# Kernel tuning notes

Measured on AMD Instinct MI355X. Metric: run time of the kernel, lower is better.

The kernel has to match this reference:

```python
import jax, jax.numpy as jnp
import numpy as np

GROUPS = 32
EPS = 1e-5


def group_norm(x, scale, bias):
    # x: [B, C, T]
    b, c, t = x.shape
    xg = x.reshape(b, GROUPS, c // GROUPS, t)
    mean = xg.mean(axis=(2, 3), keepdims=True)
    var = xg.var(axis=(2, 3), keepdims=True)
    xg = (xg - mean) * jax.lax.rsqrt(var + EPS)
    return xg.reshape(b, c, t) * scale[None, :, None] + bias[None, :, None]


def setup_inputs() -> dict:
    key = jax.random.key(0)
    ks = jax.random.split(key, 7)
    B, C, H, W = 8, 512, 32, 32
    x = jax.random.normal(ks[0], (B, C, H, W), dtype=jnp.float32)
    gn_scale = jnp.ones((C,), jnp.float32)
    gn_bias = jnp.zeros((C,), jnp.float32)
    qkv_w = jax.random.normal(ks[1], (3 * C, C), jnp.float32) / np.sqrt(C)
    qkv_b = jnp.zeros((3 * C,), jnp.float32)
    # proj_out is zero-initialized in the original; use small random weights
    # so the attention path contributes to the output (trained-model behavior).
    proj_w = jax.random.normal(ks[2], (C, C), jnp.float32) / np.sqrt(C)
    proj_b = jnp.zeros((C,), jnp.float32)
    return {"x": x, "gn_scale": gn_scale, "gn_bias": gn_bias,
            "qkv_w": qkv_w, "qkv_b": qkv_b, "proj_w": proj_w, "proj_b": proj_b}


def reference(x, gn_scale, gn_bias, qkv_w, qkv_b, proj_w, proj_b):
    NUM_HEADS = 8
    b, c, *spatial = x.shape
    t = int(np.prod(spatial))
    xf = x.reshape(b, c, t)                                   # [B,C,T]
    xn = group_norm(xf, gn_scale, gn_bias)
    qkv = jnp.einsum('oc,bct->bot', qkv_w, xn) + qkv_b[None, :, None]  # [B,3C,T]
    # legacy layout: reshape to heads BEFORE splitting into q,k,v thirds
    qkv = qkv.reshape(b * NUM_HEADS, -1, t)                   # [B*H, 3C/H, T]
    ch = qkv.shape[1] // 3
    q, k, v = jnp.split(qkv, 3, axis=1)                       # each [B*H, ch, T]
    scale = 1.0 / np.sqrt(np.sqrt(ch))
    w = jnp.einsum('bct,bcs->bts', q * scale, k * scale)      # [B*H, T, T]
    w = jax.nn.softmax(w.astype(jnp.float32), axis=-1).astype(w.dtype)
    h = jnp.einsum('bts,bcs->bct', w, v)                      # [B*H, ch, T]
    h = h.reshape(b, c, t)
    h = jnp.einsum('oc,bct->bot', proj_w, h) + proj_b[None, :, None]
    return (xf + h).reshape(b, c, *spatial)
```

## Files before the change

### kernel.cpp

```cpp
#include <hip/hip_runtime.h>

typedef __bf16 bf16;
typedef __attribute__((ext_vector_type(8))) __bf16 bf16x8;
typedef __attribute__((ext_vector_type(4))) __bf16 bf16x4;
typedef __attribute__((ext_vector_type(4))) float f32x4;

#define MFMA(a, b, c) __builtin_amdgcn_mfma_f32_16x16x32_bf16(a, b, c, 0, 0, 0)
#define GLOAD_LDS(g, l)                                                        \
  __builtin_amdgcn_global_load_lds(                                            \
      (const __attribute__((address_space(1))) void*)(g),                      \
      (__attribute__((address_space(3))) void*)(l), 16, 0, 0)

#if __has_builtin(__builtin_amdgcn_exp2f)
#define EXP2(x) __builtin_amdgcn_exp2f(x)
#else
#define EXP2(x) exp2f(x)
#endif

#define C1LOG 0.18033688011f

__device__ __forceinline__ int swz64(int row, int col) {
  return row * 64 + (col ^ ((row & 7) << 3));
}

__global__ void k_pre(const float* __restrict__ x, const float* __restrict__ gs,
                      const float* __restrict__ gb, const float* __restrict__ qw,
                      const float* __restrict__ pw, bf16* __restrict__ xnT,
                      bf16* __restrict__ wq, bf16* __restrict__ wp) {
  int tid = threadIdx.x;
  __shared__ float red[2][4];
  if (blockIdx.x >= 256) {
    int i = (blockIdx.x - 256) * 256 + tid;
    int idx = i * 4;
    float4 v;
    bf16* o;
    if (idx < 786432) {
      v = *(const float4*)(qw + idx);
      o = wq + idx;
    } else {
      int j = idx - 786432;
      v = *(const float4*)(pw + j);
      o = wp + j;
    }
    o[0] = (bf16)v.x; o[1] = (bf16)v.y; o[2] = (bf16)v.z; o[3] = (bf16)v.w;
    return;
  }
  int blk = blockIdx.x;
  int b = blk >> 5, g = blk & 31;
  const float* xp = x + ((size_t)(b * 512 + g * 16)) * 1024;
  float s = 0.f, ss = 0.f;
  for (int i = tid; i < 4096; i += 256) {
    float4 v = ((const float4*)xp)[i];
    s += v.x + v.y + v.z + v.w;
    ss += v.x * v.x + v.y * v.y + v.z * v.z + v.w * v.w;
  }
#pragma unroll
  for (int m = 1; m < 64; m <<= 1) {
    s += __shfl_xor(s, m);
    ss += __shfl_xor(ss, m);
  }
  int wid = tid >> 6;
  if ((tid & 63) == 0) { red[0][wid] = s; red[1][wid] = ss; }
  __syncthreads();
  float fs = red[0][0] + red[0][1] + red[0][2] + red[0][3];
  float fss = red[1][0] + red[1][1] + red[1][2] + red[1][3];
  float mean = fs * (1.f / 16384.f);
  float var = fss * (1.f / 16384.f) - mean * mean;
  float inv = rsqrtf(var + 1e-5f);
  float a_[16], b_[16];
#pragma unroll
  for (int cl = 0; cl < 16; ++cl) {
    float sc = gs[g * 16 + cl] * inv;
    a_[cl] = sc;
    b_[cl] = gb[g * 16 + cl] - mean * sc;
  }
  bf16* outp = xnT + (size_t)b * 1024 * 512 + g * 16;
  for (int k = 0; k < 4; ++k) {
    int t = tid + k * 256;
    __align__(16) bf16 tmp[16];
#pragma unroll
    for (int cl = 0; cl < 16; ++cl) {
      float v = xp[(size_t)cl * 1024 + t];
      tmp[cl] = (bf16)(v * a_[cl] + b_[cl]);
    }
    *(bf16x8*)(outp + (size_t)t * 512) = *(bf16x8*)tmp;
    *(bf16x8*)(outp + (size_t)t * 512 + 8) = *(bf16x8*)(tmp + 8);
  }
}

__global__ void k_qkv(const bf16* __restrict__ xnT, const bf16* __restrict__ wq,
                      const float* __restrict__ qb, bf16* __restrict__ qkvT,
                      bf16* __restrict__ vTout) {
  int bid = blockIdx.x;
  int swz = (bid & 7) * 96 + (bid >> 3);
  int nt = swz % 12, mt = swz / 12;
  int tid = threadIdx.x, lane = tid & 63;
  int wid = tid >> 6, wr = wid >> 1, wc = wid & 1;
  int lr = lane & 15, lk8 = (lane >> 4) * 8, prow4 = (lane >> 4) * 4;
  __shared__ __align__(16) bf16 lA[8192], lB[8192];
  const bf16* Ab = xnT + (size_t)mt * 128 * 512;
  const bf16* Bb = wq + (size_t)nt * 128 * 512;
  f32x4 acc[4][4] = {};
  int ubase = tid & 192;
  for (int kt = 0; kt < 8; ++kt) {
    __syncthreads();
#pragma unroll
    for (int i = 0; i < 4; ++i) {
      int s = i * 256 + tid;
      int r = s >> 3, cc = (s & 7) ^ (r & 7);
      GLOAD_LDS(Ab + (size_t)r * 512 + kt * 64 + cc * 8, lA + (i * 256 + ubase) * 8);
      GLOAD_LDS(Bb + (size_t)r * 512 + kt * 64 + cc * 8, lB + (i * 256 + ubase) * 8);
    }
    __syncthreads();
#pragma unroll
    for (int ksl = 0; ksl < 2; ++ksl) {
      bf16x8 aF[4], bF[4];
#pragma unroll
      for (int m = 0; m < 4; ++m)
        aF[m] = *(bf16x8*)&lA[swz64(wr * 64 + m * 16 + lr, ksl * 32 + lk8)];
#pragma unroll
      for (int n = 0; n < 4; ++n)
        bF[n] = *(bf16x8*)&lB[swz64(wc * 64 + n * 16 + lr, ksl * 32 + lk8)];
      __builtin_amdgcn_s_setprio(1);
#pragma unroll
      for (int m = 0; m < 4; ++m)
#pragma unroll
        for (int n = 0; n < 4; ++n) acc[m][n] = MFMA(aF[m], bF[n], acc[m][n]);
      __builtin_amdgcn_s_setprio(0);
    }
  }
#pragma unroll
  for (int n = 0; n < 4; ++n) {
    int o = nt * 128 + wc * 64 + n * 16 + lr;
    float bias = qb[o];
    int hh = o / 192;
    int om = o - hh * 192;
    bool isv = om >= 128;
    float scl = (om >= 64 && om < 128) ? C1LOG : 1.0f;
    int c = om - 128;
#pragma unroll
    for (int m = 0; m < 4; ++m) {
      int row0 = mt * 128 + wr * 64 + m * 16 + prow4;
      if (isv) {
        int bb = row0 >> 10, t0 = row0 & 1023;
        bf16x4 v4;
#pragma unroll
        for (int r = 0; r < 4; ++r) v4[r] = (bf16)(acc[m][n][r] + bias);
        *(bf16x4*)&vTout[(((size_t)bb * 8 + hh) * 64 + c) * 1024 + t0] = v4;
      } else {
#pragma unroll
        for (int r = 0; r < 4; ++r)
          qkvT[(size_t)(row0 + r) * 1536 + o] = (bf16)((acc[m][n][r] + bias) * scl);
      }
    }
  }
}

__global__ __launch_bounds__(512, 4) void k_attn(const bf16* __restrict__ qkvT,
                                                 const bf16* __restrict__ vT,
                                                 bf16* __restrict__ hT) {
  int d = blockIdx.x;
  int head = (d & 7) * 8 + (d >> 6);
  int qt = (d >> 3) & 7;
  int b = head >> 3, hh = head & 7;
  int tid = threadIdx.x, lane = tid & 63, wid = tid >> 6;
  int lr = lane & 15, hi = lane >> 4, lk8 = hi * 8;

  __shared__ __align__(16) bf16 KT[2][4096];
  __shared__ __align__(16) bf16 VTl[2][4096];
  __shared__ __align__(16) bf16 PT[8][1024];

  const bf16* qbase = qkvT + (size_t)b * 1024 * 1536 + hh * 192;
  const bf16* kbase = qbase + 64;
  const bf16* vbase = vT + (size_t)head * 64 * 1024;

  int tq = qt * 128 + wid * 16 + lr;
  bf16x8 qf0 = *(const bf16x8*)(qbase + (size_t)tq * 1536 + lk8);
  bf16x8 qf1 = *(const bf16x8*)(qbase + (size_t)tq * 1536 + 32 + lk8);

  f32x4 hacc[4] = {};
  float m2 = -1e30f, l_ = 0.f;

  int r_ = tid >> 3;
  int cc_ = (tid & 7) ^ (r_ & 7);
  const bf16* ksrc = kbase + (size_t)r_ * 1536 + cc_ * 8;
  const bf16* vsrc = vbase + (size_t)r_ * 1024 + cc_ * 8;
  int lbase = (tid >> 6) * 512;

  GLOAD_LDS(ksrc, KT[0] + lbase);
  GLOAD_LDS(vsrc, VTl[0] + lbase);

  for (int it = 0; it < 16; ++it) {
    int cur = it & 1;
    asm volatile("s_waitcnt vmcnt(0) lgkmcnt(0)" ::: "memory");
    __builtin_amdgcn_s_barrier();
    __builtin_amdgcn_sched_barrier(0);
    if (it < 15) {
      int sb = (it + 1) * 64;
      GLOAD_LDS(ksrc + (size_t)sb * 1536, KT[cur ^ 1] + lbase);
      GLOAD_LDS(vsrc + sb, VTl[cur ^ 1] + lbase);
    }
    f32x4 sc[4];
#pragma unroll
    for (int n = 0; n < 4; ++n) sc[n] = f32x4{0.f, 0.f, 0.f, 0.f};
    __builtin_amdgcn_s_setprio(1);
#pragma unroll
    for (int n = 0; n < 4; ++n) {
      bf16x8 kA0 = *(bf16x8*)&KT[cur][swz64(n * 16 + lr, lk8)];
      bf16x8 kA1 = *(bf16x8*)&KT[cur][swz64(n * 16 + lr, 32 + lk8)];
      sc[n] = MFMA(kA0, qf0, sc[n]);
      sc[n] = MFMA(kA1, qf1, sc[n]);
    }
    __builtin_amdgcn_s_setprio(0);
    float tm = fmaxf(
        fmaxf(fmaxf(fmaxf(sc[0][0], sc[0][1]), fmaxf(sc[0][2], sc[0][3])),
              fmaxf(fmaxf(sc[1][0], sc[1][1]), fmaxf(sc[1][2], sc[1][3]))),
        fmaxf(fmaxf(fmaxf(sc[2][0], sc[2][1]), fmaxf(sc[2][2], sc[2][3])),
              fmaxf(fmaxf(sc[3][0], sc[3][1]), fmaxf(sc[3][2], sc[3][3]))));
    tm = fmaxf(tm, __shfl_xor(tm, 16));
    tm = fmaxf(tm, __shfl_xor(tm, 32));
    if (__any(tm > m2 + 7.213f)) {
      float mn = fmaxf(m2, tm);
      float al = EXP2(m2 - mn);
      m2 = mn;
      l_ *= al;
#pragma unroll
      for (int n = 0; n < 4; ++n) {
        hacc[n][0] *= al; hacc[n][1] *= al; hacc[n][2] *= al; hacc[n][3] *= al;
      }
    }
    float rs = 0.f;
#pragma unroll
    for (int n = 0; n < 4; ++n) {
      float e0 = EXP2(sc[n][0] - m2), e1 = EXP2(sc[n][1] - m2);
      float e2 = EXP2(sc[n][2] - m2), e3 = EXP2(sc[n][3] - m2);
      rs += (e0 + e1) + (e2 + e3);
      bf16x4 p4;
      p4[0] = (bf16)e0; p4[1] = (bf16)e1; p4[2] = (bf16)e2; p4[3] = (bf16)e3;
      *(bf16x4*)&PT[wid][swz64(lr, n * 16 + hi * 4)] = p4;
    }
    rs += __shfl_xor(rs, 16);
    rs += __shfl_xor(rs, 32);
    l_ += rs;
    asm volatile("s_waitcnt lgkmcnt(0)" ::: "memory");
    __builtin_amdgcn_sched_barrier(0);
    bf16x8 pa0 = *(bf16x8*)&PT[wid][swz64(lr, lk8)];
    bf16x8 pa1 = *(bf16x8*)&PT[wid][swz64(lr, 32 + lk8)];
    __builtin_amdgcn_s_setprio(1);
#pragma unroll
    for (int n = 0; n < 4; ++n) {
      bf16x8 vA0 = *(bf16x8*)&VTl[cur][swz64(n * 16 + lr, lk8)];
      bf16x8 vA1 = *(bf16x8*)&VTl[cur][swz64(n * 16 + lr, 32 + lk8)];
      hacc[n] = MFMA(vA0, pa0, hacc[n]);
      hacc[n] = MFMA(vA1, pa1, hacc[n]);
    }
    __builtin_amdgcn_s_setprio(0);
  }
  float invl = 1.f / l_;
  bf16* dst = hT + ((size_t)b * 1024 + tq) * 512 + hh * 64 + hi * 4;
#pragma unroll
  for (int n = 0; n < 4; ++n) {
    bf16x4 o4;
#pragma unroll
    for (int r = 0; r < 4; ++r) o4[r] = (bf16)(hacc[n][r] * invl);
    *(bf16x4*)(dst + n * 16) = o4;
  }
}

__global__ void k_proj(const bf16* __restrict__ hT, const bf16* __restrict__ wp,
                       const float* __restrict__ pb, const float* __restrict__ x,
                       float* __restrict__ out) {
  int bid = blockIdx.x;
  int swz = (bid & 7) * 64 + (bid >> 3);
  int nt = swz & 7, mt = swz >> 3;
  int tid = threadIdx.x, lane = tid & 63;
  int wid = tid >> 6, wr = wid >> 1, wc = wid & 1;
  int lr = lane & 15, lk8 = (lane >> 4) * 8, prow4 = (lane >> 4) * 4;
  __shared__ __align__(16) bf16 lA[8192], lB[4096];
  const bf16* Ab = hT + (size_t)mt * 128 * 512;
  const bf16* Bb = wp + (size_t)nt * 64 * 512;
  f32x4 acc[4][2] = {};
  int ubase = tid & 192;
  for (int kt = 0; kt < 8; ++kt) {
    __syncthreads();
#pragma unroll
    for (int i = 0; i < 4; ++i) {
      int s = i * 256 + tid;
      int r = s >> 3, cc = (s & 7) ^ (r & 7);
      GLOAD_LDS(Ab + (size_t)r * 512 + kt * 64 + cc * 8, lA + (i * 256 + ubase) * 8);
    }
#pragma unroll
    for (int i = 0; i < 2; ++i) {
      int s = i * 256 + tid;
      int r = s >> 3, cc = (s & 7) ^ (r & 7);
      GLOAD_LDS(Bb + (size_t)r * 512 + kt * 64 + cc * 8, lB + (i * 256 + ubase) * 8);
    }
    __syncthreads();
#pragma unroll
    for (int ksl = 0; ksl < 2; ++ksl) {
      bf16x8 aF[4], bF[2];
#pragma unroll
      for (int m = 0; m < 4; ++m)
        aF[m] = *(bf16x8*)&lA[swz64(wr * 64 + m * 16 + lr, ksl * 32 + lk8)];
#pragma unroll
      for (int n = 0; n < 2; ++n)
        bF[n] = *(bf16x8*)&lB[swz64(wc * 32 + n * 16 + lr, ksl * 32 + lk8)];
      __builtin_amdgcn_s_setprio(1);
#pragma unroll
      for (int m = 0; m < 4; ++m)
#pragma unroll
        for (int n = 0; n < 2; ++n) acc[m][n] = MFMA(aF[m], bF[n], acc[m][n]);
      __builtin_amdgcn_s_setprio(0);
    }
  }
#pragma unroll
  for (int n = 0; n < 2; ++n) {
    int o = nt * 64 + wc * 32 + n * 16 + lr;
    float bias = pb[o];
#pragma unroll
    for (int m = 0; m < 4; ++m) {
      int row0 = mt * 128 + wr * 64 + m * 16 + prow4;
      int bb = row0 >> 10, t0 = row0 & 1023;
      size_t off = ((size_t)bb * 512 + o) * 1024 + t0;
      float4 xv = *(const float4*)(x + off);
      float4 rr;
      rr.x = acc[m][n][0] + xv.x + bias;
      rr.y = acc[m][n][1] + xv.y + bias;
      rr.z = acc[m][n][2] + xv.z + bias;
      rr.w = acc[m][n][3] + xv.w + bias;
      *(float4*)(out + off) = rr;
    }
  }
}

extern "C" void kernel_launch(void* const* d_in, const int* in_sizes, int n_in,
                              void* d_out, int out_size, void* d_ws, size_t ws_size,
                              hipStream_t stream) {
  const float* x = (const float*)d_in[0];
  const float* gs = (const float*)d_in[1];
  const float* gb = (const float*)d_in[2];
  const float* qw = (const float*)d_in[3];
  const float* qb = (const float*)d_in[4];
  const float* pw = (const float*)d_in[5];
  const float* pb = (const float*)d_in[6];
  float* out = (float*)d_out;
  char* ws = (char*)d_ws;
  bf16* xnT  = (bf16*)(ws);
  bf16* qkvT = (bf16*)(ws + 8388608);
  bf16* vT   = (bf16*)(ws + 33554432);
  bf16* hT   = (bf16*)(ws + 41943040);
  bf16* wq   = (bf16*)(ws + 50331648);
  bf16* wp   = (bf16*)(ws + 51904512);

  k_pre<<<1280, 256, 0, stream>>>(x, gs, gb, qw, pw, xnT, wq, wp);
  k_qkv<<<768, 256, 0, stream>>>(xnT, wq, qb, qkvT, vT);
  k_attn<<<512, 512, 0, stream>>>(qkvT, vT, hT);
  k_proj<<<512, 256, 0, stream>>>(hT, wp, pb, x, out);
}
```

Baseline: 78.08 us.

## Triple-buffer K/V loads in attention and stage group-norm input through LDS

```diff
diff --git a/kernel.cpp b/kernel.cpp
--- a/kernel.cpp
+++ b/kernel.cpp
@@ -23,12 +23,12 @@
   return row * 64 + (col ^ ((row & 7) << 3));
 }
 
-__global__ void k_pre(const float* __restrict__ x, const float* __restrict__ gs,
-                      const float* __restrict__ gb, const float* __restrict__ qw,
-                      const float* __restrict__ pw, bf16* __restrict__ xnT,
-                      bf16* __restrict__ wq, bf16* __restrict__ wp) {
+__global__ __launch_bounds__(256, 2) void k_pre(
+    const float* __restrict__ x, const float* __restrict__ gs,
+    const float* __restrict__ gb, const float* __restrict__ qw,
+    const float* __restrict__ pw, bf16* __restrict__ xnT,
+    bf16* __restrict__ wq, bf16* __restrict__ wp) {
   int tid = threadIdx.x;
-  __shared__ float red[2][4];
   if (blockIdx.x >= 256) {
     int i = (blockIdx.x - 256) * 256 + tid;
     int idx = i * 4;
@@ -45,12 +45,15 @@
     o[0] = (bf16)v.x; o[1] = (bf16)v.y; o[2] = (bf16)v.z; o[3] = (bf16)v.w;
     return;
   }
+  __shared__ float xs[16 * 1024];
+  __shared__ float red[2][4];
   int blk = blockIdx.x;
   int b = blk >> 5, g = blk & 31;
   const float* xp = x + ((size_t)(b * 512 + g * 16)) * 1024;
   float s = 0.f, ss = 0.f;
   for (int i = tid; i < 4096; i += 256) {
     float4 v = ((const float4*)xp)[i];
+    *(float4*)&xs[i * 4] = v;
     s += v.x + v.y + v.z + v.w;
     ss += v.x * v.x + v.y * v.y + v.z * v.z + v.w * v.w;
   }
@@ -74,17 +77,21 @@
     a_[cl] = sc;
     b_[cl] = gb[g * 16 + cl] - mean * sc;
   }
+  int t0 = tid * 4;
+  bf16 tmp[4][16];
+#pragma unroll
+  for (int cl = 0; cl < 16; ++cl) {
+    float4 v = *(float4*)&xs[cl * 1024 + t0];
+    tmp[0][cl] = (bf16)(v.x * a_[cl] + b_[cl]);
+    tmp[1][cl] = (bf16)(v.y * a_[cl] + b_[cl]);
+    tmp[2][cl] = (bf16)(v.z * a_[cl] + b_[cl]);
+    tmp[3][cl] = (bf16)(v.w * a_[cl] + b_[cl]);
+  }
   bf16* outp = xnT + (size_t)b * 1024 * 512 + g * 16;
+#pragma unroll
   for (int k = 0; k < 4; ++k) {
-    int t = tid + k * 256;
-    __align__(16) bf16 tmp[16];
-#pragma unroll
-    for (int cl = 0; cl < 16; ++cl) {
-      float v = xp[(size_t)cl * 1024 + t];
-      tmp[cl] = (bf16)(v * a_[cl] + b_[cl]);
-    }
-    *(bf16x8*)(outp + (size_t)t * 512) = *(bf16x8*)tmp;
-    *(bf16x8*)(outp + (size_t)t * 512 + 8) = *(bf16x8*)(tmp + 8);
+    *(bf16x8*)(outp + (size_t)(t0 + k) * 512) = *(bf16x8*)&tmp[k][0];
+    *(bf16x8*)(outp + (size_t)(t0 + k) * 512 + 8) = *(bf16x8*)&tmp[k][8];
   }
 }
 
@@ -166,8 +173,8 @@
   int tid = threadIdx.x, lane = tid & 63, wid = tid >> 6;
   int lr = lane & 15, hi = lane >> 4, lk8 = hi * 8;
 
-  __shared__ __align__(16) bf16 KT[2][4096];
-  __shared__ __align__(16) bf16 VTl[2][4096];
+  __shared__ __align__(16) bf16 KT[3][4096];
+  __shared__ __align__(16) bf16 VTl[3][4096];
   __shared__ __align__(16) bf16 PT[8][1024];
 
   const bf16* qbase = qkvT + (size_t)b * 1024 * 1536 + hh * 192;
@@ -189,16 +196,22 @@
 
   GLOAD_LDS(ksrc, KT[0] + lbase);
   GLOAD_LDS(vsrc, VTl[0] + lbase);
+  GLOAD_LDS(ksrc + (size_t)64 * 1536, KT[1] + lbase);
+  GLOAD_LDS(vsrc + 64, VTl[1] + lbase);
 
   for (int it = 0; it < 16; ++it) {
-    int cur = it & 1;
-    asm volatile("s_waitcnt vmcnt(0) lgkmcnt(0)" ::: "memory");
+    int cur = it % 3;
+    if (it < 15)
+      asm volatile("s_waitcnt vmcnt(2)" ::: "memory");
+    else
+      asm volatile("s_waitcnt vmcnt(0)" ::: "memory");
     __builtin_amdgcn_s_barrier();
     __builtin_amdgcn_sched_barrier(0);
-    if (it < 15) {
-      int sb = (it + 1) * 64;
-      GLOAD_LDS(ksrc + (size_t)sb * 1536, KT[cur ^ 1] + lbase);
-      GLOAD_LDS(vsrc + sb, VTl[cur ^ 1] + lbase);
+    if (it < 14) {
+      int sb = (it + 2) * 64;
+      int nx = (it + 2) % 3;
+      GLOAD_LDS(ksrc + (size_t)sb * 1536, KT[nx] + lbase);
+      GLOAD_LDS(vsrc + sb, VTl[nx] + lbase);
     }
     f32x4 sc[4];
 #pragma unroll
```

Measured after the change: 76.82 us. About the same (-1.6%).
